# Kernel optimization log

Hardware: AMD Instinct MI355X
Metric: run time of the kernel (lower is better)

Reference implementation:

```python
import jax, jax.numpy as jnp
import numpy as np

N = 100000   # nodes
E = 600000   # edges
G = 64       # graphs in batch
H = 128      # hidden size
F_NODE = 2
F_EDGE = 7
RH = 500     # reghead size
NEG_SLOPE = 0.01
BN_EPS = 1e-5


def leaky(x):
    return jnp.where(x >= 0, x, NEG_SLOPE * x)


def gine_conv(x, src, dst, edge_attr, edge_W, edge_b, W1, b1, gamma, beta, W2, b2):
    # PyG GINEConv: message = ReLU(x_j + Lin(edge_attr)); sum-aggregate at dst;
    # out = nn((1+eps)*x + aggr) with eps=0; nn = Lin -> BN(train) -> LeakyReLU -> Lin -> LeakyReLU
    e = edge_attr @ edge_W.T + edge_b                 # [E, d_in]
    m = jax.nn.relu(x[src] + e)                       # gather + add + relu
    aggr = jax.ops.segment_sum(m, dst, num_segments=N)
    h = x + aggr
    h = h @ W1.T + b1                                 # [N, H]
    mu = jnp.mean(h, axis=0)
    var = jnp.var(h, axis=0)                          # biased, matches BN training
    h = gamma * (h - mu) * jax.lax.rsqrt(var + BN_EPS) + beta
    h = leaky(h)
    h = h @ W2.T + b2
    return leaky(h)


def setup_inputs() -> dict:
    key = jax.random.key(0)
    ks = jax.random.split(key, 24)

    def lin(k, out_d, in_d):
        s = 1.0 / np.sqrt(in_d)
        k1, k2 = jax.random.split(k)
        return (jax.random.uniform(k1, (out_d, in_d), jnp.float32, -s, s),
                jax.random.uniform(k2, (out_d,), jnp.float32, -s, s))

    x = jax.random.normal(ks[0], (N, F_NODE), jnp.float32)
    edge_index = jax.random.randint(ks[1], (2, E), 0, N, jnp.int32)
    batch = jnp.sort(jax.random.randint(ks[2], (N,), 0, G, jnp.int32))
    edge_attr = jax.random.normal(ks[3], (E, F_EDGE), jnp.float32)

    # layer 0 (in_dim = F_NODE)
    ew0, eb0 = lin(ks[4], F_NODE, F_EDGE)
    w10, b10 = lin(ks[5], H, F_NODE)
    g0, be0 = jnp.ones((H,), jnp.float32), jnp.zeros((H,), jnp.float32)
    w20, b20 = lin(ks[6], H, H)

    # 3 hidden layers, stacked (in_dim = H)
    L = 3
    ewS = jnp.stack([lin(ks[7 + i], H, F_EDGE)[0] for i in range(L)])
    ebS = jnp.stack([lin(jax.random.fold_in(ks[7 + i], 1), H, F_EDGE)[1] for i in range(L)])
    w1S = jnp.stack([lin(ks[10 + i], H, H)[0] for i in range(L)])
    b1S = jnp.stack([lin(jax.random.fold_in(ks[10 + i], 1), H, H)[1] for i in range(L)])
    gS = jnp.ones((L, H), jnp.float32)
    beS = jnp.zeros((L, H), jnp.float32)
    w2S = jnp.stack([lin(ks[13 + i], H, H)[0] for i in range(L)])
    b2S = jnp.stack([lin(jax.random.fold_in(ks[13 + i], 1), H, H)[1] for i in range(L)])

    wr, br = lin(ks[16], RH, H)
    we, be_ = lin(ks[17], 1, RH)

    return {"x": x, "edge_index": edge_index, "batch": batch, "edge_attr": edge_attr,
            "ew0": ew0, "eb0": eb0, "w10": w10, "b10": b10, "g0": g0, "be0": be0,
            "w20": w20, "b20": b20,
            "ewS": ewS, "ebS": ebS, "w1S": w1S, "b1S": b1S, "gS": gS, "beS": beS,
            "w2S": w2S, "b2S": b2S, "wr": wr, "br": br, "we": we, "be_": be_}


def reference(x, edge_index, batch, edge_attr,
              ew0, eb0, w10, b10, g0, be0, w20, b20,
              ewS, ebS, w1S, b1S, gS, beS, w2S, b2S,
              wr, br, we, be_):
    src, dst = edge_index[0], edge_index[1]
    h = gine_conv(x, src, dst, edge_attr, ew0, eb0, w10, b10, g0, be0, w20, b20)
    h = leaky(h)  # outer self.relu; dropout p=0 is identity
    for i in range(ewS.shape[0]):
        h = gine_conv(h, src, dst, edge_attr, ewS[i], ebS[i], w1S[i], b1S[i],
                      gS[i], beS[i], w2S[i], b2S[i])
        h = leaky(h)
    # global_mean_pool
    sums = jax.ops.segment_sum(h, batch, num_segments=G)
    cnt = jax.ops.segment_sum(jnp.ones((h.shape[0],), h.dtype), batch, num_segments=G)
    pooled = sums / jnp.maximum(cnt, 1.0)[:, None]
    # reghead_layers == 2
    r = leaky(pooled @ wr.T + br)
    return r @ we.T + be_
```

## Files before the change

kernel.cpp:

```cpp
#include <hip/hip_runtime.h>

#define NNODES 100000
#define NEDGES 600000
#define NGRAPH 64
#define HID 128
#define RHD 500
#define NB ((NNODES + 255) / 256)
#define EB ((NEDGES + 255) / 256)
#define GG ((NNODES + 63) / 64)

typedef __attribute__((ext_vector_type(8))) short short8;
typedef __attribute__((ext_vector_type(4))) float f32x4;

__device__ __forceinline__ float leaky1(float x) { return x >= 0.0f ? x : 0.01f * x; }

__device__ __forceinline__ void splitf(float a, unsigned short& h, unsigned short& l)
{
    unsigned u = __float_as_uint(a);
    unsigned r = (u + 0x7FFFu + ((u >> 16) & 1u)) & 0xFFFF0000u;
    h = (unsigned short)(r >> 16);
    float res = a - __uint_as_float(r);
    unsigned u2 = __float_as_uint(res);
    l = (unsigned short)((u2 + 0x7FFFu + ((u2 >> 16) & 1u)) >> 16);
}

__global__ __launch_bounds__(256) void hist_kernel(
    const int* __restrict__ ei, int* __restrict__ deg)
{
    int e = blockIdx.x * 256 + threadIdx.x;
    if (e < NEDGES) atomicAdd(&deg[ei[NEDGES + e]], 1);
}

__global__ __launch_bounds__(256) void scan_blk(
    const int* __restrict__ deg, int* __restrict__ incl, int* __restrict__ bsum)
{
    __shared__ int s[256];
    int t = threadIdx.x;
    int n = blockIdx.x * 256 + t;
    int v = (n < NNODES) ? deg[n] : 0;
    int x = v;
    s[t] = x;
    __syncthreads();
    for (int off = 1; off < 256; off <<= 1) {
        int y = (t >= off) ? s[t - off] : 0;
        __syncthreads();
        x += y; s[t] = x;
        __syncthreads();
    }
    if (n < NNODES) incl[n] = x;
    if (t == 255) bsum[blockIdx.x] = x;
}

__global__ __launch_bounds__(512) void scan_bsum(int* __restrict__ bsum, int nblk)
{
    __shared__ int s[512];
    int t = threadIdx.x;
    int v = (t < nblk) ? bsum[t] : 0;
    int x = v;
    s[t] = x;
    __syncthreads();
    for (int off = 1; off < 512; off <<= 1) {
        int y = (t >= off) ? s[t - off] : 0;
        __syncthreads();
        x += y; s[t] = x;
        __syncthreads();
    }
    if (t < nblk) bsum[t] = x - v;
}

__global__ __launch_bounds__(256) void finalize_rp(
    const int* __restrict__ deg, const int* __restrict__ bsum,
    int* __restrict__ rp, int* __restrict__ cursor)
{
    int n = blockIdx.x * 256 + threadIdx.x;
    if (n >= NNODES) return;
    int ig = rp[n] + bsum[blockIdx.x];
    int st = ig - deg[n];
    rp[n] = st;
    cursor[n] = st;
    if (n == NNODES - 1) rp[NNODES] = ig;
}

__global__ __launch_bounds__(256) void scatter_kernel(
    const int* __restrict__ ei, int* __restrict__ cursor, int* __restrict__ eid)
{
    int e = blockIdx.x * 256 + threadIdx.x;
    if (e >= NEDGES) return;
    int d = ei[NEDGES + e];
    int pos = atomicAdd(&cursor[d], 1);
    eid[pos] = e;
}

__global__ __launch_bounds__(256) void seg_sort(
    const int* __restrict__ rp, int* __restrict__ eid)
{
    int n = blockIdx.x * 256 + threadIdx.x;
    if (n >= NNODES) return;
    int beg = rp[n], end = rp[n + 1];
    for (int i = beg + 1; i < end; ++i) {
        int key = eid[i];
        int j = i - 1;
        while (j >= beg && eid[j] > key) { eid[j + 1] = eid[j]; --j; }
        eid[j + 1] = key;
    }
}

__global__ __launch_bounds__(256) void permute_kernel(
    const int* __restrict__ eid, const int* __restrict__ ei,
    const float* __restrict__ ea, int* __restrict__ srcp, float* __restrict__ eap)
{
    int p = blockIdx.x * 256 + threadIdx.x;
    if (p >= NEDGES) return;
    int id = eid[p];
    srcp[p] = ei[id];
    const float* s = ea + (size_t)id * 7;
    float* d = eap + (size_t)p * 7;
#pragma unroll
    for (int k = 0; k < 7; ++k) d[k] = s[k];
}

__global__ __launch_bounds__(256) void wsplit_all(
    const float* __restrict__ w20, const float* __restrict__ w1S,
    const float* __restrict__ w2S,
    unsigned short* __restrict__ wh, unsigned short* __restrict__ wl)
{
    int i = blockIdx.x * 256 + threadIdx.x;
    int m = i >> 14;
    int off = i & 16383;
    const float* src;
    if (m == 0) src = w20;
    else if (m <= 3) src = w1S + (size_t)(m - 1) * 16384;
    else src = w2S + (size_t)(m - 4) * 16384;
    unsigned short h, l;
    splitf(src[off], h, l);
    wh[i] = h;
    wl[i] = l;
}

__global__ __launch_bounds__(256) void aggregate0_kernel(
    const float* __restrict__ x, const int* __restrict__ rp,
    const int* __restrict__ srcp, const float* __restrict__ eap,
    const float* __restrict__ ew, const float* __restrict__ eb,
    float* __restrict__ aggr2)
{
    int n = blockIdx.x * 256 + threadIdx.x;
    if (n >= NNODES) return;
    float w0[7], w1[7];
#pragma unroll
    for (int k = 0; k < 7; ++k) { w0[k] = ew[k]; w1[k] = ew[7 + k]; }
    float e0b = eb[0], e1b = eb[1];
    float a0 = x[n * 2 + 0], a1 = x[n * 2 + 1];
    int beg = rp[n], end = rp[n + 1];
    for (int e = beg; e < end; ++e) {
        int s = srcp[e];
        const float* ap = eap + (size_t)e * 7;
        float t0 = e0b, t1 = e1b;
#pragma unroll
        for (int k = 0; k < 7; ++k) {
            float av = ap[k];
            t0 = fmaf(av, w0[k], t0);
            t1 = fmaf(av, w1[k], t1);
        }
        a0 += fmaxf(x[s * 2 + 0] + t0, 0.0f);
        a1 += fmaxf(x[s * 2 + 1] + t1, 0.0f);
    }
    aggr2[n * 2 + 0] = a0;
    aggr2[n * 2 + 1] = a1;
}

__global__ __launch_bounds__(256) void aggregate_kernel(
    const float* __restrict__ hin, const int* __restrict__ rp,
    const int* __restrict__ srcp, const float* __restrict__ eap,
    const float* __restrict__ ew, const float* __restrict__ eb,
    unsigned short* __restrict__ Ahi, unsigned short* __restrict__ Alo)
{
    int lane = threadIdx.x & 63;
    int w = threadIdx.x >> 6;
    int nbase = blockIdx.x * 32 + w * 8;
    const int c0 = 2 * lane, c1 = 2 * lane + 1;
    float ew0[7], ew1[7];
#pragma unroll
    for (int k = 0; k < 7; ++k) {
        ew0[k] = ew[c0 * 7 + k];
        ew1[k] = ew[c1 * 7 + k];
    }
    float eb0v = eb[c0], eb1v = eb[c1];
    for (int n = nbase; n < nbase + 8; ++n) {
        float2 av = ((const float2*)(hin + (size_t)n * HID))[lane];
        float a0 = av.x, a1 = av.y;
        int beg = rp[n], end = rp[n + 1];
        int e = beg;
        for (; e + 4 <= end; e += 4) {
            int s0 = srcp[e], s1 = srcp[e + 1], s2 = srcp[e + 2], s3 = srcp[e + 3];
            const float* ap = eap + (size_t)e * 7;
            float2 x0 = ((const float2*)(hin + (size_t)s0 * HID))[lane];
            float2 x1 = ((const float2*)(hin + (size_t)s1 * HID))[lane];
            float2 x2 = ((const float2*)(hin + (size_t)s2 * HID))[lane];
            float2 x3 = ((const float2*)(hin + (size_t)s3 * HID))[lane];
            float t00 = eb0v, t01 = eb1v, t10 = eb0v, t11 = eb1v;
            float t20 = eb0v, t21 = eb1v, t30 = eb0v, t31 = eb1v;
#pragma unroll
            for (int k = 0; k < 7; ++k) {
                float av0 = ap[k], av1 = ap[7 + k], av2 = ap[14 + k], av3 = ap[21 + k];
                t00 = fmaf(av0, ew0[k], t00); t01 = fmaf(av0, ew1[k], t01);
                t10 = fmaf(av1, ew0[k], t10); t11 = fmaf(av1, ew1[k], t11);
                t20 = fmaf(av2, ew0[k], t20); t21 = fmaf(av2, ew1[k], t21);
                t30 = fmaf(av3, ew0[k], t30); t31 = fmaf(av3, ew1[k], t31);
            }
            a0 += fmaxf(x0.x + t00, 0.0f);
            a1 += fmaxf(x0.y + t01, 0.0f);
            a0 += fmaxf(x1.x + t10, 0.0f);
            a1 += fmaxf(x1.y + t11, 0.0f);
            a0 += fmaxf(x2.x + t20, 0.0f);
            a1 += fmaxf(x2.y + t21, 0.0f);
            a0 += fmaxf(x3.x + t30, 0.0f);
            a1 += fmaxf(x3.y + t31, 0.0f);
        }
        for (; e < end; ++e) {
            int s = srcp[e];
            const float* ap = eap + (size_t)e * 7;
            float2 xv = ((const float2*)(hin + (size_t)s * HID))[lane];
            float t0 = eb0v, t1 = eb1v;
#pragma unroll
            for (int k = 0; k < 7; ++k) {
                float av = ap[k];
                t0 = fmaf(av, ew0[k], t0);
                t1 = fmaf(av, ew1[k], t1);
            }
            a0 += fmaxf(xv.x + t0, 0.0f);
            a1 += fmaxf(xv.y + t1, 0.0f);
        }
        unsigned short h0, l0, h1v, l1v;
        splitf(a0, h0, l0);
        splitf(a1, h1v, l1v);
        size_t rb = (size_t)n * HID;
        ((unsigned*)(Ahi + rb))[lane] = (unsigned)h0 | ((unsigned)h1v << 16);
        ((unsigned*)(Alo + rb))[lane] = (unsigned)l0 | ((unsigned)l1v << 16);
    }
}

__global__ __launch_bounds__(256) void gemm1_l0_kernel(
    const float* __restrict__ aggr2,
    const float* __restrict__ w1, const float* __restrict__ b1,
    float* __restrict__ h1)
{
    int n = blockIdx.x * 256 + threadIdx.x;
    if (n >= NNODES) return;
    float x0 = aggr2[n * 2 + 0];
    float x1 = aggr2[n * 2 + 1];
    float4* out4 = (float4*)(h1 + (size_t)n * HID);
    for (int j = 0; j < HID; j += 4) {
        float4 o;
        o.x = fmaf(x1, w1[(j + 0) * 2 + 1], fmaf(x0, w1[(j + 0) * 2 + 0], b1[j + 0]));
        o.y = fmaf(x1, w1[(j + 1) * 2 + 1], fmaf(x0, w1[(j + 1) * 2 + 0], b1[j + 1]));
        o.z = fmaf(x1, w1[(j + 2) * 2 + 1], fmaf(x0, w1[(j + 2) * 2 + 0], b1[j + 2]));
        o.w = fmaf(x1, w1[(j + 3) * 2 + 1], fmaf(x0, w1[(j + 3) * 2 + 0], b1[j + 3]));
        out4[j >> 2] = o;
    }
}

__global__ __launch_bounds__(256) void bn_stats_part(
    const float* __restrict__ h1, float* __restrict__ part)
{
    __shared__ float ls[HID], lq[HID];
    int c = threadIdx.x & 127;
    int half = threadIdx.x >> 7;
    int base = blockIdx.x * 256;
    int end = base + 256; if (end > NNODES) end = NNODES;
    float s = 0.0f, q = 0.0f;
    for (int r = base + half; r < end; r += 2) {
        float v = h1[(size_t)r * HID + c];
        s += v;
        q = fmaf(v, v, q);
    }
    if (half) { ls[c] = s; lq[c] = q; }
    __syncthreads();
    if (!half) {
        s += ls[c]; q += lq[c];
        part[(size_t)blockIdx.x * 256 + c] = s;
        part[(size_t)blockIdx.x * 256 + 128 + c] = q;
    }
}

__global__ __launch_bounds__(256) void bn_finalize(
    const float* __restrict__ part, int nblk,
    const float* __restrict__ gamma, const float* __restrict__ beta,
    float* __restrict__ scsh)
{
    __shared__ float ls[256], lq[256];
    int c = blockIdx.x;
    int t = threadIdx.x;
    float s = 0.0f, q = 0.0f;
    for (int i = t; i < nblk; i += 256) {
        s += part[(size_t)i * 256 + c];
        q += part[(size_t)i * 256 + 128 + c];
    }
    ls[t] = s; lq[t] = q;
    __syncthreads();
#pragma unroll
    for (int off = 128; off >= 1; off >>= 1) {
        if (t < off) { ls[t] += ls[t + off]; lq[t] += lq[t + off]; }
        __syncthreads();
    }
    if (t == 0) {
        const float invN = 1.0f / (float)NNODES;
        float mu = ls[0] * invN;
        float var = fmaf(-mu, mu, lq[0] * invN);
        float iv = rsqrtf(var + 1e-5f);
        float sc = gamma[c] * iv;
        scsh[c] = sc;
        scsh[HID + c] = beta[c] - mu * sc;
    }
}

__global__ __launch_bounds__(256) void gemm1_lds(
    const unsigned short* __restrict__ Ahi, const unsigned short* __restrict__ Alo,
    const unsigned short* __restrict__ wh, const unsigned short* __restrict__ wl,
    const float* __restrict__ b1, float* __restrict__ h1,
    float* __restrict__ part)
{
    __shared__ __align__(16) short lds[16384];
    const int t = threadIdx.x;
    const int mb = blockIdx.x * 64;

#pragma unroll
    for (int u = 0; u < 4; ++u) {
        int idx = u * 256 + t;
        int row = idx >> 4, sl = idx & 15;
        int gr = mb + row;
        short8 hv, lv;
#pragma unroll
        for (int e = 0; e < 8; ++e) { hv[e] = 0; lv[e] = 0; }
        if (gr < NNODES) {
            hv = *(const short8*)(Ahi + (size_t)gr * HID + sl * 8);
            lv = *(const short8*)(Alo + (size_t)gr * HID + sl * 8);
        }
        int byt = row * 256 + ((sl ^ (row & 7)) << 4);
        *(short8*)((char*)lds + byt) = hv;
        *(short8*)((char*)lds + 16384 + byt) = lv;
    }
    __syncthreads();

    const int lane = t & 63;
    const int wv = t >> 6;
    const int cl = lane & 15, g = lane >> 4, x = lane & 7;
    const int colbase = wv * 32;

    int aoff[4];
#pragma unroll
    for (int ks = 0; ks < 4; ++ks)
        aoff[ks] = cl * 256 + (((ks * 4 + g) ^ x) << 4);

    const unsigned short* wb_h0 = wh + (size_t)(colbase + cl) * HID + g * 8;
    const unsigned short* wb_h1 = wb_h0 + 16 * HID;
    const unsigned short* wb_l0 = wl + (size_t)(colbase + cl) * HID + g * 8;
    const unsigned short* wb_l1 = wb_l0 + 16 * HID;

    f32x4 acc[4][2];
#pragma unroll
    for (int rt = 0; rt < 4; ++rt) {
        acc[rt][0] = (f32x4){0.f, 0.f, 0.f, 0.f};
        acc[rt][1] = (f32x4){0.f, 0.f, 0.f, 0.f};
    }

#pragma unroll
    for (int ks = 0; ks < 4; ++ks) {
        short8 bh0 = *(const short8*)(wb_h0 + ks * 32);
        short8 bh1 = *(const short8*)(wb_h1 + ks * 32);
        short8 bl0 = *(const short8*)(wb_l0 + ks * 32);
        short8 bl1 = *(const short8*)(wb_l1 + ks * 32);
#pragma unroll
        for (int rt = 0; rt < 4; ++rt) {
            short8 ah = *(const short8*)((const char*)lds + (rt * 4096) + aoff[ks]);
            short8 al = *(const short8*)((const char*)lds + (16384 + rt * 4096) + aoff[ks]);
            acc[rt][0] = __builtin_amdgcn_mfma_f32_16x16x32_bf16(ah, bh0, acc[rt][0], 0, 0, 0);
            acc[rt][1] = __builtin_amdgcn_mfma_f32_16x16x32_bf16(ah, bh1, acc[rt][1], 0, 0, 0);
            acc[rt][0] = __builtin_amdgcn_mfma_f32_16x16x32_bf16(al, bh0, acc[rt][0], 0, 0, 0);
            acc[rt][1] = __builtin_amdgcn_mfma_f32_16x16x32_bf16(al, bh1, acc[rt][1], 0, 0, 0);
            acc[rt][0] = __builtin_amdgcn_mfma_f32_16x16x32_bf16(ah, bl0, acc[rt][0], 0, 0, 0);
            acc[rt][1] = __builtin_amdgcn_mfma_f32_16x16x32_bf16(ah, bl1, acc[rt][1], 0, 0, 0);
        }
    }

    float bj0 = b1[colbase + cl];
    float bj1 = b1[colbase + 16 + cl];
    float s0 = 0.f, q0 = 0.f, s1 = 0.f, q1 = 0.f;
#pragma unroll
    for (int rt = 0; rt < 4; ++rt) {
        int rbase = mb + rt * 16 + g * 4;
#pragma unroll
        for (int r = 0; r < 4; ++r) {
            int grow = rbase + r;
            if (grow < NNODES) {
                float o0 = acc[rt][0][r] + bj0;
                float o1 = acc[rt][1][r] + bj1;
                h1[(size_t)grow * HID + colbase + cl] = o0;
                h1[(size_t)grow * HID + colbase + 16 + cl] = o1;
                s0 += o0; q0 = fmaf(o0, o0, q0);
                s1 += o1; q1 = fmaf(o1, o1, q1);
            }
        }
    }
    __syncthreads();
    float* red = (float*)lds;
    red[(colbase + cl) * 4 + g] = s0;
    red[(colbase + 16 + cl) * 4 + g] = s1;
    red[512 + (colbase + cl) * 4 + g] = q0;
    red[512 + (colbase + 16 + cl) * 4 + g] = q1;
    __syncthreads();
    {
        int stat = t >> 7, col = t & 127;
        const float* bp = red + stat * 512 + col * 4;
        part[(size_t)blockIdx.x * 256 + stat * 128 + col] = bp[0] + bp[1] + bp[2] + bp[3];
    }
}

template<int PRE, int POST>
__global__ __launch_bounds__(256) void gemm_mfma(
    const float* __restrict__ Ain, const float* __restrict__ scsh,
    const unsigned short* __restrict__ wh, const unsigned short* __restrict__ wl,
    const float* __restrict__ bias, float* __restrict__ Hout)
{
    __shared__ __align__(16) short lds[16384];
    const int t = threadIdx.x;
    const int mb = blockIdx.x * 64;

    const float4* sc4 = (const float4*)scsh;
    const float4* sh4 = (const float4*)(scsh + HID);

#pragma unroll
    for (int u = 0; u < 4; ++u) {
        int idx = u * 256 + t;
        int row = idx >> 4, sl = idx & 15;
        float4 v0 = make_float4(0.f, 0.f, 0.f, 0.f);
        float4 v1 = make_float4(0.f, 0.f, 0.f, 0.f);
        int gr = mb + row;
        if (gr < NNODES) {
            const float4* p = (const float4*)(Ain + (size_t)gr * HID + sl * 8);
            v0 = p[0]; v1 = p[1];
            if (PRE) {
                float4 c0 = sc4[sl * 2], c1 = sc4[sl * 2 + 1];
                float4 s0 = sh4[sl * 2], s1 = sh4[sl * 2 + 1];
                v0.x = leaky1(fmaf(v0.x, c0.x, s0.x));
                v0.y = leaky1(fmaf(v0.y, c0.y, s0.y));
                v0.z = leaky1(fmaf(v0.z, c0.z, s0.z));
                v0.w = leaky1(fmaf(v0.w, c0.w, s0.w));
                v1.x = leaky1(fmaf(v1.x, c1.x, s1.x));
                v1.y = leaky1(fmaf(v1.y, c1.y, s1.y));
                v1.z = leaky1(fmaf(v1.z, c1.z, s1.z));
                v1.w = leaky1(fmaf(v1.w, c1.w, s1.w));
            }
        }
        unsigned short h[8], l[8];
        splitf(v0.x, h[0], l[0]); splitf(v0.y, h[1], l[1]);
        splitf(v0.z, h[2], l[2]); splitf(v0.w, h[3], l[3]);
        splitf(v1.x, h[4], l[4]); splitf(v1.y, h[5], l[5]);
        splitf(v1.z, h[6], l[6]); splitf(v1.w, h[7], l[7]);
        short8 hv, lv;
#pragma unroll
        for (int e = 0; e < 8; ++e) { hv[e] = (short)h[e]; lv[e] = (short)l[e]; }
        int byt = row * 256 + ((sl ^ (row & 7)) << 4);
        *(short8*)((char*)lds + byt) = hv;
        *(short8*)((char*)lds + 16384 + byt) = lv;
    }
    __syncthreads();

    const int lane = t & 63;
    const int wv = t >> 6;
    const int cl = lane & 15, g = lane >> 4, x = lane & 7;
    const int colbase = wv * 32;

    int aoff[4];
#pragma unroll
    for (int ks = 0; ks < 4; ++ks)
        aoff[ks] = cl * 256 + (((ks * 4 + g) ^ x) << 4);

    const unsigned short* wb_h0 = wh + (size_t)(colbase + cl) * HID + g * 8;
    const unsigned short* wb_h1 = wb_h0 + 16 * HID;
    const unsigned short* wb_l0 = wl + (size_t)(colbase + cl) * HID + g * 8;
    const unsigned short* wb_l1 = wb_l0 + 16 * HID;

    f32x4 acc[4][2];
#pragma unroll
    for (int rt = 0; rt < 4; ++rt) {
        acc[rt][0] = (f32x4){0.f, 0.f, 0.f, 0.f};
        acc[rt][1] = (f32x4){0.f, 0.f, 0.f, 0.f};
    }

#pragma unroll
    for (int ks = 0; ks < 4; ++ks) {
        short8 bh0 = *(const short8*)(wb_h0 + ks * 32);
        short8 bh1 = *(const short8*)(wb_h1 + ks * 32);
        short8 bl0 = *(const short8*)(wb_l0 + ks * 32);
        short8 bl1 = *(const short8*)(wb_l1 + ks * 32);
#pragma unroll
        for (int rt = 0; rt < 4; ++rt) {
            short8 ah = *(const short8*)((const char*)lds + (rt * 4096) + aoff[ks]);
            short8 al = *(const short8*)((const char*)lds + (16384 + rt * 4096) + aoff[ks]);
            acc[rt][0] = __builtin_amdgcn_mfma_f32_16x16x32_bf16(ah, bh0, acc[rt][0], 0, 0, 0);
            acc[rt][1] = __builtin_amdgcn_mfma_f32_16x16x32_bf16(ah, bh1, acc[rt][1], 0, 0, 0);
            acc[rt][0] = __builtin_amdgcn_mfma_f32_16x16x32_bf16(al, bh0, acc[rt][0], 0, 0, 0);
            acc[rt][1] = __builtin_amdgcn_mfma_f32_16x16x32_bf16(al, bh1, acc[rt][1], 0, 0, 0);
            acc[rt][0] = __builtin_amdgcn_mfma_f32_16x16x32_bf16(ah, bl0, acc[rt][0], 0, 0, 0);
            acc[rt][1] = __builtin_amdgcn_mfma_f32_16x16x32_bf16(ah, bl1, acc[rt][1], 0, 0, 0);
        }
    }

    float bj0 = bias[colbase + cl];
    float bj1 = bias[colbase + 16 + cl];
#pragma unroll
    for (int rt = 0; rt < 4; ++rt) {
        int rbase = mb + rt * 16 + g * 4;
#pragma unroll
        for (int r = 0; r < 4; ++r) {
            int grow = rbase + r;
            if (grow < NNODES) {
                float o0 = acc[rt][0][r] + bj0;
                float o1 = acc[rt][1][r] + bj1;
                if (POST) { o0 = leaky1(leaky1(o0)); o1 = leaky1(leaky1(o1)); }
                Hout[(size_t)grow * HID + colbase + cl] = o0;
                Hout[(size_t)grow * HID + colbase + 16 + cl] = o1;
            }
        }
    }
}

__global__ __launch_bounds__(256) void pool_kernel(
    const float* __restrict__ h, const int* __restrict__ batch,
    float* __restrict__ sums, float* __restrict__ cnt)
{
    int c = threadIdx.x & 127;
    int half = threadIdx.x >> 7;
    int base = blockIdx.x * 128 + half * 64;
    if (base >= NNODES) return;
    int end = base + 64; if (end > NNODES) end = NNODES;
    int g = batch[base];
    float acc = 0.0f, k = 0.0f;
    for (int n = base; n < end; ++n) {
        int gn = batch[n];
        if (gn != g) {
            atomicAdd(&sums[g * HID + c], acc);
            if (c == 0) atomicAdd(&cnt[g], k);
            acc = 0.0f; k = 0.0f; g = gn;
        }
        acc += h[(size_t)n * HID + c];
        k += 1.0f;
    }
    atomicAdd(&sums[g * HID + c], acc);
    if (c == 0) atomicAdd(&cnt[g], k);
}

__global__ __launch_bounds__(512) void reghead_kernel(
    const float* __restrict__ sums, const float* __restrict__ cnt,
    const float* __restrict__ wr, const float* __restrict__ br,
    const float* __restrict__ we, const float* __restrict__ be,
    float* __restrict__ out)
{
    __shared__ float pool[8 * HID];
    __shared__ float red[8][8];
    int g0 = blockIdx.x * 8;
    for (int i = threadIdx.x; i < 8 * HID; i += 512) {
        int g = g0 + (i >> 7);
        float c = cnt[g]; c = fmaxf(c, 1.0f);
        pool[i] = sums[g * HID + (i & 127)] / c;
    }
    __syncthreads();
    int j = threadIdx.x;
    float p[8];
#pragma unroll
    for (int g = 0; g < 8; ++g) p[g] = 0.0f;
    if (j < RHD) {
        float accs[8];
        float bjv = br[j];
#pragma unroll
        for (int g = 0; g < 8; ++g) accs[g] = bjv;
        const float4* wr4 = (const float4*)(wr + (size_t)j * HID);
        const float4* pool4 = (const float4*)pool;
        for (int k = 0; k < 32; ++k) {
            float4 w = wr4[k];
#pragma unroll
            for (int g = 0; g < 8; ++g) {
                float4 pv = pool4[g * 32 + k];
                accs[g] = fmaf(w.x, pv.x, accs[g]);
                accs[g] = fmaf(w.y, pv.y, accs[g]);
                accs[g] = fmaf(w.z, pv.z, accs[g]);
                accs[g] = fmaf(w.w, pv.w, accs[g]);
            }
        }
        float wej = we[j];
#pragma unroll
        for (int g = 0; g < 8; ++g) p[g] = leaky1(accs[g]) * wej;
    }
    int lane = threadIdx.x & 63, wid = threadIdx.x >> 6;
#pragma unroll
    for (int g = 0; g < 8; ++g) {
        float v = p[g];
        v += __shfl_down(v, 32); v += __shfl_down(v, 16); v += __shfl_down(v, 8);
        v += __shfl_down(v, 4);  v += __shfl_down(v, 2);  v += __shfl_down(v, 1);
        if (lane == 0) red[g][wid] = v;
    }
    __syncthreads();
    if (threadIdx.x < 8) {
        float sv = be[0];
#pragma unroll
        for (int w = 0; w < 8; ++w) sv += red[threadIdx.x][w];
        out[g0 + threadIdx.x] = sv;
    }
}

extern "C" void kernel_launch(void* const* d_in, const int* in_sizes, int n_in,
                              void* d_out, int out_size, void* d_ws, size_t ws_size,
                              hipStream_t stream)
{
    const float* x     = (const float*)d_in[0];
    const int*   ei    = (const int*)d_in[1];
    const int*   batch = (const int*)d_in[2];
    const float* ea    = (const float*)d_in[3];
    const float* ew0   = (const float*)d_in[4];
    const float* eb0   = (const float*)d_in[5];
    const float* w10   = (const float*)d_in[6];
    const float* b10   = (const float*)d_in[7];
    const float* g0v   = (const float*)d_in[8];
    const float* be0   = (const float*)d_in[9];
    const float* w20   = (const float*)d_in[10];
    const float* b20   = (const float*)d_in[11];
    const float* ewS   = (const float*)d_in[12];
    const float* ebS   = (const float*)d_in[13];
    const float* w1S   = (const float*)d_in[14];
    const float* b1S   = (const float*)d_in[15];
    const float* gS    = (const float*)d_in[16];
    const float* beS   = (const float*)d_in[17];
    const float* w2S   = (const float*)d_in[18];
    const float* b2S   = (const float*)d_in[19];
    const float* wr    = (const float*)d_in[20];
    const float* br    = (const float*)d_in[21];
    const float* we    = (const float*)d_in[22];
    const float* be_   = (const float*)d_in[23];

    float* ws    = (float*)d_ws;
    float* buf0  = ws;
    float* buf1  = buf0 + (size_t)NNODES * HID;
    float* buf2  = buf1 + (size_t)NNODES * HID;
    unsigned short* Ahi = (unsigned short*)buf2;
    unsigned short* Alo = Ahi + (size_t)NNODES * HID;
    float* part  = buf2 + (size_t)NNODES * HID;
    float* scsh  = part + (size_t)GG * 256;
    float* sums  = scsh + 256;
    float* cnt   = sums + NGRAPH * HID;
    float* aggr2 = cnt + NGRAPH;
    float* eap   = aggr2 + (size_t)NNODES * 2;
    int*   deg    = (int*)(eap + (size_t)NEDGES * 7);
    int*   cursor = deg + NNODES;
    int*   bsum   = cursor + NNODES;
    int*   rp     = bsum + 512;
    int*   eid    = rp + NNODES + 1;
    int*   srcp   = eid + NEDGES;
    unsigned short* whA = (unsigned short*)(srcp + NEDGES);
    unsigned short* wlA = whA + 7 * 16384;
    float* out   = (float*)d_out;

    hipMemsetAsync(deg, 0, (size_t)NNODES * sizeof(int), stream);
    hist_kernel<<<EB, 256, 0, stream>>>(ei, deg);
    scan_blk<<<NB, 256, 0, stream>>>(deg, rp, bsum);
    scan_bsum<<<1, 512, 0, stream>>>(bsum, NB);
    finalize_rp<<<NB, 256, 0, stream>>>(deg, bsum, rp, cursor);
    scatter_kernel<<<EB, 256, 0, stream>>>(ei, cursor, eid);
    seg_sort<<<NB, 256, 0, stream>>>(rp, eid);
    permute_kernel<<<EB, 256, 0, stream>>>(eid, ei, ea, srcp, eap);

    wsplit_all<<<448, 256, 0, stream>>>(w20, w1S, w2S, whA, wlA);

    aggregate0_kernel<<<NB, 256, 0, stream>>>(x, rp, srcp, eap, ew0, eb0, aggr2);
    gemm1_l0_kernel<<<NB, 256, 0, stream>>>(aggr2, w10, b10, buf0);
    bn_stats_part<<<NB, 256, 0, stream>>>(buf0, part);
    bn_finalize<<<HID, 256, 0, stream>>>(part, NB, g0v, be0, scsh);
    gemm_mfma<1, 1><<<GG, 256, 0, stream>>>(buf0, scsh, whA, wlA, b20, buf1);

    for (int i = 0; i < 3; ++i) {
        aggregate_kernel<<<NNODES / 32, 256, 0, stream>>>(buf1, rp, srcp, eap,
            ewS + (size_t)i * HID * 7, ebS + (size_t)i * HID, Ahi, Alo);
        gemm1_lds<<<GG, 256, 0, stream>>>(Ahi, Alo,
            whA + (size_t)(1 + i) * 16384, wlA + (size_t)(1 + i) * 16384,
            b1S + (size_t)i * HID, buf0, part);
        bn_finalize<<<HID, 256, 0, stream>>>(part, GG,
            gS + (size_t)i * HID, beS + (size_t)i * HID, scsh);
        gemm_mfma<1, 1><<<GG, 256, 0, stream>>>(buf0, scsh,
            whA + (size_t)(4 + i) * 16384, wlA + (size_t)(4 + i) * 16384,
            b2S + (size_t)i * HID, buf1);
    }

    hipMemsetAsync(sums, 0, (size_t)(NGRAPH * HID + NGRAPH) * sizeof(float), stream);
    pool_kernel<<<(NNODES + 127) / 128, 256, 0, stream>>>(buf1, batch, sums, cnt);
    reghead_kernel<<<NGRAPH / 8, 512, 0, stream>>>(sums, cnt, wr, br, we, be_, out);
}
```

Before: 688.2 us.

## Stream edges across node boundaries in aggregation, one channel per lane

The hidden-layer aggregation kernel now assigns each lane a single channel, with two waves sharing a group of 8 nodes. Each wave walks the group's combined edge range in chunks of 4 and emits a node's result whenever the edge index crosses a row-pointer boundary. The intent is to keep the 4-wide unrolled gather busy across low-degree nodes instead of falling into a per-node remainder loop, and to double the number of waves. In exchange, gathers shrink from float2 to scalar loads, stores become 16-bit scalar, and inner while loops add branching that can diverge.

```diff
diff --git a/kernel.cpp b/kernel.cpp
--- a/kernel.cpp
+++ b/kernel.cpp
@@ -174,68 +174,80 @@
     const float* __restrict__ ew, const float* __restrict__ eb,
     unsigned short* __restrict__ Ahi, unsigned short* __restrict__ Alo)
 {
-    int lane = threadIdx.x & 63;
-    int w = threadIdx.x >> 6;
-    int nbase = blockIdx.x * 32 + w * 8;
-    const int c0 = 2 * lane, c1 = 2 * lane + 1;
-    float ew0[7], ew1[7];
-#pragma unroll
-    for (int k = 0; k < 7; ++k) {
-        ew0[k] = ew[c0 * 7 + k];
-        ew1[k] = ew[c1 * 7 + k];
-    }
-    float eb0v = eb[c0], eb1v = eb[c1];
-    for (int n = nbase; n < nbase + 8; ++n) {
-        float2 av = ((const float2*)(hin + (size_t)n * HID))[lane];
-        float a0 = av.x, a1 = av.y;
-        int beg = rp[n], end = rp[n + 1];
-        int e = beg;
-        for (; e + 4 <= end; e += 4) {
-            int s0 = srcp[e], s1 = srcp[e + 1], s2 = srcp[e + 2], s3 = srcp[e + 3];
-            const float* ap = eap + (size_t)e * 7;
-            float2 x0 = ((const float2*)(hin + (size_t)s0 * HID))[lane];
-            float2 x1 = ((const float2*)(hin + (size_t)s1 * HID))[lane];
-            float2 x2 = ((const float2*)(hin + (size_t)s2 * HID))[lane];
-            float2 x3 = ((const float2*)(hin + (size_t)s3 * HID))[lane];
-            float t00 = eb0v, t01 = eb1v, t10 = eb0v, t11 = eb1v;
-            float t20 = eb0v, t21 = eb1v, t30 = eb0v, t31 = eb1v;
-#pragma unroll
-            for (int k = 0; k < 7; ++k) {
-                float av0 = ap[k], av1 = ap[7 + k], av2 = ap[14 + k], av3 = ap[21 + k];
-                t00 = fmaf(av0, ew0[k], t00); t01 = fmaf(av0, ew1[k], t01);
-                t10 = fmaf(av1, ew0[k], t10); t11 = fmaf(av1, ew1[k], t11);
-                t20 = fmaf(av2, ew0[k], t20); t21 = fmaf(av2, ew1[k], t21);
-                t30 = fmaf(av3, ew0[k], t30); t31 = fmaf(av3, ew1[k], t31);
-            }
-            a0 += fmaxf(x0.x + t00, 0.0f);
-            a1 += fmaxf(x0.y + t01, 0.0f);
-            a0 += fmaxf(x1.x + t10, 0.0f);
-            a1 += fmaxf(x1.y + t11, 0.0f);
-            a0 += fmaxf(x2.x + t20, 0.0f);
-            a1 += fmaxf(x2.y + t21, 0.0f);
-            a0 += fmaxf(x3.x + t30, 0.0f);
-            a1 += fmaxf(x3.y + t31, 0.0f);
-        }
-        for (; e < end; ++e) {
-            int s = srcp[e];
-            const float* ap = eap + (size_t)e * 7;
-            float2 xv = ((const float2*)(hin + (size_t)s * HID))[lane];
-            float t0 = eb0v, t1 = eb1v;
-#pragma unroll
-            for (int k = 0; k < 7; ++k) {
-                float av = ap[k];
-                t0 = fmaf(av, ew0[k], t0);
-                t1 = fmaf(av, ew1[k], t1);
-            }
-            a0 += fmaxf(xv.x + t0, 0.0f);
-            a1 += fmaxf(xv.y + t1, 0.0f);
-        }
-        unsigned short h0, l0, h1v, l1v;
-        splitf(a0, h0, l0);
-        splitf(a1, h1v, l1v);
-        size_t rb = (size_t)n * HID;
-        ((unsigned*)(Ahi + rb))[lane] = (unsigned)h0 | ((unsigned)h1v << 16);
-        ((unsigned*)(Alo + rb))[lane] = (unsigned)l0 | ((unsigned)l1v << 16);
+    const int lane = threadIdx.x & 63;
+    const int w = threadIdx.x >> 6;
+    const int grp = w >> 1, half = w & 1;
+    const int nbase = blockIdx.x * 16 + grp * 8;
+    const int nend = nbase + 8;
+    const int c = half * 64 + lane;
+
+    float ewv[7];
+#pragma unroll
+    for (int k = 0; k < 7; ++k) ewv[k] = ew[c * 7 + k];
+    const float ebv = eb[c];
+
+    int n = nbase;
+    int e = rp[nbase];
+    const int eend = rp[nend];
+    int next = rp[n + 1];
+    float a = hin[(size_t)n * HID + c];
+
+#define EMIT_ADVANCE() { \
+        unsigned short hh, ll; splitf(a, hh, ll); \
+        size_t rb = (size_t)n * HID + c; \
+        Ahi[rb] = hh; Alo[rb] = ll; \
+        ++n; a = hin[(size_t)n * HID + c]; next = rp[n + 1]; }
+
+    while (e + 4 <= eend) {
+        int s0 = srcp[e], s1 = srcp[e + 1], s2 = srcp[e + 2], s3 = srcp[e + 3];
+        const float* ap = eap + (size_t)e * 7;
+        float x0 = hin[(size_t)s0 * HID + c];
+        float x1 = hin[(size_t)s1 * HID + c];
+        float x2 = hin[(size_t)s2 * HID + c];
+        float x3 = hin[(size_t)s3 * HID + c];
+        float t0 = ebv, t1 = ebv, t2 = ebv, t3 = ebv;
+#pragma unroll
+        for (int k = 0; k < 7; ++k) {
+            t0 = fmaf(ap[k],      ewv[k], t0);
+            t1 = fmaf(ap[7 + k],  ewv[k], t1);
+            t2 = fmaf(ap[14 + k], ewv[k], t2);
+            t3 = fmaf(ap[21 + k], ewv[k], t3);
+        }
+        float m0 = fmaxf(x0 + t0, 0.0f);
+        float m1 = fmaxf(x1 + t1, 0.0f);
+        float m2 = fmaxf(x2 + t2, 0.0f);
+        float m3 = fmaxf(x3 + t3, 0.0f);
+        while (e >= next)     EMIT_ADVANCE();
+        a += m0;
+        while (e + 1 >= next) EMIT_ADVANCE();
+        a += m1;
+        while (e + 2 >= next) EMIT_ADVANCE();
+        a += m2;
+        while (e + 3 >= next) EMIT_ADVANCE();
+        a += m3;
+        e += 4;
+    }
+    for (; e < eend; ++e) {
+        int s = srcp[e];
+        const float* ap = eap + (size_t)e * 7;
+        float xv = hin[(size_t)s * HID + c];
+        float t = ebv;
+#pragma unroll
+        for (int k = 0; k < 7; ++k) t = fmaf(ap[k], ewv[k], t);
+        while (e >= next) EMIT_ADVANCE();
+        a += fmaxf(xv + t, 0.0f);
+    }
+#undef EMIT_ADVANCE
+    while (n < nend) {
+        unsigned short hh, ll;
+        splitf(a, hh, ll);
+        size_t rb = (size_t)n * HID + c;
+        Ahi[rb] = hh; Alo[rb] = ll;
+        ++n;
+        if (n < nend) {
+            a = hin[(size_t)n * HID + c];
+            next = rp[n + 1];
+        }
     }
 }
 
@@ -677,7 +689,7 @@
     gemm_mfma<1, 1><<<GG, 256, 0, stream>>>(buf0, scsh, whA, wlA, b20, buf1);
 
     for (int i = 0; i < 3; ++i) {
-        aggregate_kernel<<<NNODES / 32, 256, 0, stream>>>(buf1, rp, srcp, eap,
+        aggregate_kernel<<<NNODES / 16, 256, 0, stream>>>(buf1, rp, srcp, eap,
             ewS + (size_t)i * HID * 7, ebS + (size_t)i * HID, Ahi, Alo);
         gemm1_lds<<<GG, 256, 0, stream>>>(Ahi, Alo,
             whA + (size_t)(1 + i) * 16384, wlA + (size_t)(1 + i) * 16384,
```

Measured after the change: 741.2 us. 1.08x slower.
